# Kernel tuning notes

Measured on AMD Instinct MI355X. Metric: run time of the kernel, lower is better.

Reference implementation:

```python
import jax, jax.numpy as jnp
import numpy as np

B, S, D = 4, 2048, 1024
H, DK, DV = 16, 64, 64


def setup_inputs() -> dict:
    key = jax.random.key(0)
    ks = jax.random.split(key, 9)
    std = 1.0 / np.sqrt(D)
    inp = {
        "x": jax.random.normal(ks[0], (B, S, D), jnp.float32),
        "c": jax.random.normal(ks[1], (B, S, D), jnp.float32),
        "Wq_x": jax.random.normal(ks[2], (D, H * DK), jnp.float32) * std,
        "Wk_x": jax.random.normal(ks[3], (D, H * DK), jnp.float32) * std,
        "Wv_x": jax.random.normal(ks[4], (D, H * DV), jnp.float32) * std,
        "Wq_c": jax.random.normal(ks[5], (D, H * DK), jnp.float32) * std,
        "Wk_c": jax.random.normal(ks[6], (D, H * DK), jnp.float32) * std,
        "Wv_c": jax.random.normal(ks[7], (D, H * DV), jnp.float32) * std,
        "W_proj": jax.random.normal(ks[8], (2 * H * DV, D), jnp.float32) * (1.0 / np.sqrt(2 * H * DV)),
        "b_proj": jnp.zeros((D,), jnp.float32),
    }
    return inp


def _heads(t, hd):
    # [B,S,H*hd] -> [B,H,S,hd]
    b, s, _ = t.shape
    return t.reshape(b, s, H, hd).transpose(0, 2, 1, 3)


def reference(x, c, Wq_x, Wk_x, Wv_x, Wq_c, Wk_c, Wv_c, W_proj, b_proj):
    q = jnp.concatenate([_heads(x @ Wq_x, DK), _heads(c @ Wq_c, DK)], axis=-1)  # [B,H,S,2DK]
    k = jnp.concatenate([_heads(x @ Wk_x, DK), _heads(c @ Wk_c, DK)], axis=-1)
    v = jnp.concatenate([_heads(x @ Wv_x, DV), _heads(c @ Wv_c, DV)], axis=-1)  # [B,H,S,2DV]
    # NOTE: original scales by sqrt(k_dim), not sqrt(2*k_dim) (faithful)
    scores = jnp.einsum("bhqd,bhkd->bhqk", q, k) / np.float32(np.sqrt(DK))
    attn = jax.nn.softmax(scores, axis=-1)
    out = jnp.einsum("bhqk,bhkd->bhqd", attn, v)  # [B,H,S,2DV]
    out = out.transpose(0, 2, 1, 3).reshape(x.shape[0], x.shape[1], -1)  # [B,S,H*2DV]
    return out @ W_proj + b_proj
```

## Files before the change

kernel.cpp:

```cpp
#include <hip/hip_runtime.h>
#include <hip/hip_bf16.h>
#include <stdint.h>

#define BB 4
#define SS 2048
#define DD 1024
#define HH 16
#define DHH 128

typedef __bf16 bf16x8 __attribute__((ext_vector_type(8)));
typedef __bf16 bf16x4 __attribute__((ext_vector_type(4)));
typedef float  f32x4  __attribute__((ext_vector_type(4)));

#define GLOAD_LDS16(gp, lp) \
  __builtin_amdgcn_global_load_lds((const __attribute__((address_space(1))) unsigned int*)(gp), \
                                   (__attribute__((address_space(3))) unsigned int*)(lp), 16, 0, 0)

__global__ void cast2_kernel(const float* __restrict__ x, const float* __restrict__ c,
                             __bf16* __restrict__ out, int n) {
    int i = (blockIdx.x * blockDim.x + threadIdx.x) * 4;
    const float* src = (i < n) ? (x + i) : (c + (i - n));
    f32x4 v = *(const f32x4*)src;
    bf16x4 o;
    o[0] = (__bf16)v[0]; o[1] = (__bf16)v[1]; o[2] = (__bf16)v[2]; o[3] = (__bf16)v[3];
    *(bf16x4*)(out + i) = o;
}

__global__ void transpose_cast_kernel(const float* __restrict__ in, __bf16* __restrict__ out,
                                      int K, int N) {
    __shared__ float tile[32][33];
    int n0 = blockIdx.x * 32, k0 = blockIdx.y * 32;
    int tx = threadIdx.x, ty = threadIdx.y;
    #pragma unroll
    for (int i = 0; i < 32; i += 8)
        tile[ty + i][tx] = in[(size_t)(k0 + ty + i) * N + n0 + tx];
    __syncthreads();
    #pragma unroll
    for (int i = 0; i < 32; i += 8)
        out[(size_t)(n0 + ty + i) * K + k0 + tx] = (__bf16)tile[tx][ty + i];
}

__global__ void transpose6_kernel(const float* s0, const float* s1, const float* s2,
                                  const float* s3, const float* s4, const float* s5,
                                  __bf16* __restrict__ dst) {
    const float* srcs[6] = {s0, s1, s2, s3, s4, s5};
    const float* __restrict__ in = srcs[blockIdx.z];
    __bf16* __restrict__ out = dst + (size_t)blockIdx.z * 1024 * 1024;
    __shared__ float tile[32][33];
    int n0 = blockIdx.x * 32, k0 = blockIdx.y * 32;
    int tx = threadIdx.x, ty = threadIdx.y;
    #pragma unroll
    for (int i = 0; i < 32; i += 8)
        tile[ty + i][tx] = in[(size_t)(k0 + ty + i) * 1024 + n0 + tx];
    __syncthreads();
    #pragma unroll
    for (int i = 0; i < 32; i += 8)
        out[(size_t)(n0 + ty + i) * 1024 + k0 + tx] = (__bf16)tile[tx][ty + i];
}

template <int EPI>
__global__ void gemm128_kernel(const __bf16* __restrict__ A, const __bf16* __restrict__ Bt,
                               int K, void* __restrict__ outp, int qkv_off,
                               const float* __restrict__ bias) {
    __shared__ __bf16 As[128][32];
    __shared__ __bf16 Bs[128][32];
    const int t = threadIdx.x;
    const int wave = t >> 6, lane = t & 63;
    const int l15 = lane & 15, quad = lane >> 4;
    const int wm = (wave & 1) * 64, wn = (wave >> 1) * 64;
    const int m0 = blockIdx.x * 128, n0 = blockIdx.y * 128;
    const int lrow = lane >> 2;
    const int lcol = (lane & 3) * 8;

    f32x4 acc[4][4] = {};

    for (int k0 = 0; k0 < K; k0 += 32) {
        #pragma unroll
        for (int c2 = 0; c2 < 2; ++c2) {
            int rb = (wave * 2 + c2) * 16;
            GLOAD_LDS16(A  + (size_t)(m0 + rb + lrow) * K + k0 + lcol, &As[rb][0]);
            GLOAD_LDS16(Bt + (size_t)(n0 + rb + lrow) * K + k0 + lcol, &Bs[rb][0]);
        }
        __syncthreads();
        bf16x8 af[4], bfv[4];
        #pragma unroll
        for (int i = 0; i < 4; ++i) af[i]  = *(const bf16x8*)&As[wm + i * 16 + l15][quad * 8];
        #pragma unroll
        for (int i = 0; i < 4; ++i) bfv[i] = *(const bf16x8*)&Bs[wn + i * 16 + l15][quad * 8];
        #pragma unroll
        for (int mi = 0; mi < 4; ++mi)
            #pragma unroll
            for (int ni = 0; ni < 4; ++ni)
                acc[mi][ni] = __builtin_amdgcn_mfma_f32_16x16x32_bf16(af[mi], bfv[ni], acc[mi][ni], 0, 0, 0);
        __syncthreads();
    }

    #pragma unroll
    for (int mi = 0; mi < 4; ++mi) {
        #pragma unroll
        for (int ni = 0; ni < 4; ++ni) {
            #pragma unroll
            for (int rr = 0; rr < 4; ++rr) {
                int m = m0 + wm + mi * 16 + quad * 4 + rr;
                int n = n0 + wn + ni * 16 + l15;
                if (EPI == 0) {
                    int b = m >> 11, s = m & (SS - 1);
                    int h = n >> 6,  d = (n & 63) + qkv_off;
                    __bf16* q = (__bf16*)outp;
                    q[(((size_t)b * HH + h) * SS + s) * DHH + d] = (__bf16)acc[mi][ni][rr];
                } else if (EPI == 1) {
                    float* o = (float*)outp;
                    o[(size_t)m * 1024 + n] = acc[mi][ni][rr] + bias[n];
                } else if (EPI == 2) {
                    int h = m >> 6, dl = m & 63;
                    int b = n >> 11, s = n & (SS - 1);
                    __bf16* vt = (__bf16*)outp;
                    vt[(((size_t)b * HH + h) * DHH + dl + qkv_off) * SS + s] = (__bf16)acc[mi][ni][rr];
                } else {
                    int b = m >> 11, s = m & (SS - 1);
                    int h = n >> 6,  d = (n & 63) + qkv_off;
                    int dsw = (((d >> 3) ^ (s & 15)) << 3) | (d & 7);
                    __bf16* kq = (__bf16*)outp;
                    kq[(((size_t)b * HH + h) * SS + s) * DHH + dsw] = (__bf16)acc[mi][ni][rr];
                }
            }
        }
    }
}

#define LDS_VT 16384
#define LDS_PS 32768
__global__ __launch_bounds__(256, 2)
void attn_kernel(const __bf16* __restrict__ Q, const __bf16* __restrict__ Kg,
                 const __bf16* __restrict__ Vg, __bf16* __restrict__ O) {
    __shared__ __align__(16) char smem[49152];

    const int t = threadIdx.x;
    const int wave = t >> 6, lane = t & 63;
    const int l15 = lane & 15, quad = lane >> 4;
    const int bh = blockIdx.y;
    const int b = bh >> 4, h = bh & 15;
    const int mt = blockIdx.x;
    const size_t base  = (size_t)bh * SS * DHH;
    const size_t vbase = (size_t)bh * DHH * SS;

    int kaddr[4];
    #pragma unroll
    for (int kst = 0; kst < 4; ++kst)
        kaddr[kst] = l15 * 256 + (((4 * kst + quad) ^ l15) & 15) * 16;
    int vaddr[2];
    #pragma unroll
    for (int kst = 0; kst < 2; ++kst)
        vaddr[kst] = LDS_VT + l15 * 128 + (((4 * kst + quad) ^ (l15 & 7)) & 7) * 16;
    int prad[2];
    #pragma unroll
    for (int kst = 0; kst < 2; ++kst)
        prad[kst] = LDS_PS + (wave * 32 + l15) * 128 + (((4 * kst + quad) ^ (2 * (l15 >> 2))) & 7) * 16;
    int pwad[4];
    #pragma unroll
    for (int ns = 0; ns < 4; ++ns)
        pwad[ns] = LDS_PS + (wave * 32 + quad * 4) * 128 +
                   (((2 * ns + (l15 >> 3)) ^ (2 * quad)) & 7) * 16 + (l15 & 7) * 2;

    const __bf16* kstage = Kg + base + (size_t)wave * 2048 + lane * 8;
    const __bf16* vstage = Vg + vbase + (size_t)(wave * 32 + (lane >> 3)) * SS
                           + ((lane & 7) ^ ((lane >> 3) & 7)) * 8;

    bf16x8 qf[2][4];
    #pragma unroll
    for (int ms = 0; ms < 2; ++ms) {
        int row = mt * 128 + wave * 32 + ms * 16 + l15;
        #pragma unroll
        for (int kst = 0; kst < 4; ++kst)
            qf[ms][kst] = *(const bf16x8*)(Q + base + (size_t)row * DHH + kst * 32 + quad * 8);
    }

    f32x4 oacc[2][8] = {};
    float li_[2][4] = {};

    const float SL2E = 0.125f * 1.44269504088896f;

    for (int kt = 0; kt < SS / 64; ++kt) {
        #pragma unroll
        for (int i = 0; i < 4; ++i)
            GLOAD_LDS16(kstage + (size_t)kt * 8192 + i * 512,
                        smem + wave * 4096 + i * 1024);
        #pragma unroll
        for (int i = 0; i < 4; ++i)
            GLOAD_LDS16(vstage + kt * 64 + (size_t)i * 8 * SS,
                        smem + LDS_VT + wave * 4096 + i * 1024);
        __syncthreads();

        f32x4 sc[2][4] = {};
        #pragma unroll
        for (int kst = 0; kst < 4; ++kst) {
            bf16x8 kf[4];
            #pragma unroll
            for (int ns = 0; ns < 4; ++ns)
                kf[ns] = *(const bf16x8*)(smem + kaddr[kst] + 4096 * ns);
            #pragma unroll
            for (int ms = 0; ms < 2; ++ms)
                #pragma unroll
                for (int ns = 0; ns < 4; ++ns)
                    sc[ms][ns] = __builtin_amdgcn_mfma_f32_16x16x32_bf16(qf[ms][kst], kf[ns], sc[ms][ns], 0, 0, 0);
        }

        #pragma unroll
        for (int ms = 0; ms < 2; ++ms)
            #pragma unroll
            for (int ns = 0; ns < 4; ++ns)
                #pragma unroll
                for (int rr = 0; rr < 4; ++rr) {
                    float p = exp2f(sc[ms][ns][rr] * SL2E);
                    li_[ms][rr] += p;
                    *(__bf16*)(smem + pwad[ns] + 2048 * ms + 128 * rr) = (__bf16)p;
                }

        #pragma unroll
        for (int kst = 0; kst < 2; ++kst) {
            bf16x8 pa[2];
            #pragma unroll
            for (int ms = 0; ms < 2; ++ms)
                pa[ms] = *(const bf16x8*)(smem + prad[kst] + 2048 * ms);
            #pragma unroll
            for (int ds = 0; ds < 8; ++ds) {
                bf16x8 vf = *(const bf16x8*)(smem + vaddr[kst] + 2048 * ds);
                #pragma unroll
                for (int ms = 0; ms < 2; ++ms)
                    oacc[ms][ds] = __builtin_amdgcn_mfma_f32_16x16x32_bf16(pa[ms], vf, oacc[ms][ds], 0, 0, 0);
            }
        }
        __syncthreads();
    }

    #pragma unroll
    for (int ms = 0; ms < 2; ++ms)
        #pragma unroll
        for (int rr = 0; rr < 4; ++rr) {
            float v = li_[ms][rr];
            v += __shfl_xor(v, 1);
            v += __shfl_xor(v, 2);
            v += __shfl_xor(v, 4);
            v += __shfl_xor(v, 8);
            li_[ms][rr] = 1.f / v;
        }

    #pragma unroll
    for (int ms = 0; ms < 2; ++ms)
        #pragma unroll
        for (int rr = 0; rr < 4; ++rr) {
            int s = mt * 128 + wave * 32 + ms * 16 + quad * 4 + rr;
            size_t ob = ((size_t)b * SS + s) * (HH * DHH) + (size_t)h * DHH;
            #pragma unroll
            for (int ds = 0; ds < 8; ++ds)
                O[ob + ds * 16 + l15] = (__bf16)(oacc[ms][ds][rr] * li_[ms][rr]);
        }
}

extern "C" void kernel_launch(void* const* d_in, const int* in_sizes, int n_in,
                              void* d_out, int out_size, void* d_ws, size_t ws_size,
                              hipStream_t stream) {
    const float* x      = (const float*)d_in[0];
    const float* c      = (const float*)d_in[1];
    const float* Wq_x   = (const float*)d_in[2];
    const float* Wk_x   = (const float*)d_in[3];
    const float* Wv_x   = (const float*)d_in[4];
    const float* Wq_c   = (const float*)d_in[5];
    const float* Wk_c   = (const float*)d_in[6];
    const float* Wv_c   = (const float*)d_in[7];
    const float* W_proj = (const float*)d_in[8];
    const float* b_proj = (const float*)d_in[9];

    const size_t nXC  = (size_t)BB * SS * DD;
    const size_t nW   = (size_t)DD * DD;
    const size_t nWP  = (size_t)(2 * HH * 64) * DD;
    const size_t nQKV = (size_t)BB * HH * SS * DHH;

    __bf16* ws  = (__bf16*)d_ws;
    __bf16* xb  = ws;
    __bf16* cb  = xb + nXC;
    __bf16* wt0 = cb + nXC;
    __bf16* wt1 = wt0 + nW;
    __bf16* wt2 = wt1 + nW;
    __bf16* wt3 = wt2 + nW;
    __bf16* wt4 = wt3 + nW;
    __bf16* wt5 = wt4 + nW;
    __bf16* wtp = wt5 + nW;
    __bf16* Qb  = wtp + nWP;
    __bf16* Kb  = Qb + nQKV;
    __bf16* Vb  = Kb + nQKV;
    __bf16* Ob  = xb;

    cast2_kernel<<<(int)(2 * nXC / 1024), 256, 0, stream>>>(x, c, xb, (int)nXC);

    transpose6_kernel<<<dim3(32, 32, 6), dim3(32, 8), 0, stream>>>(
        Wq_x, Wk_x, Wv_x, Wq_c, Wk_c, Wv_c, wt0);
    transpose_cast_kernel<<<dim3(32, 64), dim3(32, 8), 0, stream>>>(W_proj, wtp, 2048, 1024);

    dim3 gg(64, 8);
    gemm128_kernel<0><<<gg, 256, 0, stream>>>(xb, wt0, 1024, Qb, 0,  nullptr);
    gemm128_kernel<0><<<gg, 256, 0, stream>>>(cb, wt3, 1024, Qb, 64, nullptr);
    gemm128_kernel<3><<<gg, 256, 0, stream>>>(xb, wt1, 1024, Kb, 0,  nullptr);
    gemm128_kernel<3><<<gg, 256, 0, stream>>>(cb, wt4, 1024, Kb, 64, nullptr);
    dim3 gv(8, 64);
    gemm128_kernel<2><<<gv, 256, 0, stream>>>(wt2, xb, 1024, Vb, 0,  nullptr);
    gemm128_kernel<2><<<gv, 256, 0, stream>>>(wt5, cb, 1024, Vb, 64, nullptr);

    attn_kernel<<<dim3(16, 64), 256, 0, stream>>>(Qb, Kb, Vb, Ob);

    gemm128_kernel<1><<<dim3(64, 8), 256, 0, stream>>>(Ob, wtp, 2048, d_out, 0, b_proj);
}
```

Before: 556.0 us.

## Fuse Q and K projections into one GEMM, prescale Q, shrink attention LDS

```diff
diff --git a/kernel.cpp b/kernel.cpp
--- a/kernel.cpp
+++ b/kernel.cpp
@@ -11,6 +11,8 @@
 typedef __bf16 bf16x8 __attribute__((ext_vector_type(8)));
 typedef __bf16 bf16x4 __attribute__((ext_vector_type(4)));
 typedef float  f32x4  __attribute__((ext_vector_type(4)));
+
+#define SL2E 0.180336880111186f
 
 #define GLOAD_LDS16(gp, lp) \
   __builtin_amdgcn_global_load_lds((const __attribute__((address_space(1))) unsigned int*)(gp), \
@@ -95,6 +97,7 @@
         __syncthreads();
     }
 
+    const size_t nQKV = (size_t)BB * HH * SS * DHH;
     #pragma unroll
     for (int mi = 0; mi < 4; ++mi) {
         #pragma unroll
@@ -103,12 +106,7 @@
             for (int rr = 0; rr < 4; ++rr) {
                 int m = m0 + wm + mi * 16 + quad * 4 + rr;
                 int n = n0 + wn + ni * 16 + l15;
-                if (EPI == 0) {
-                    int b = m >> 11, s = m & (SS - 1);
-                    int h = n >> 6,  d = (n & 63) + qkv_off;
-                    __bf16* q = (__bf16*)outp;
-                    q[(((size_t)b * HH + h) * SS + s) * DHH + d] = (__bf16)acc[mi][ni][rr];
-                } else if (EPI == 1) {
+                if (EPI == 1) {
                     float* o = (float*)outp;
                     o[(size_t)m * 1024 + n] = acc[mi][ni][rr] + bias[n];
                 } else if (EPI == 2) {
@@ -118,10 +116,16 @@
                     vt[(((size_t)b * HH + h) * DHH + dl + qkv_off) * SS + s] = (__bf16)acc[mi][ni][rr];
                 } else {
                     int b = m >> 11, s = m & (SS - 1);
-                    int h = n >> 6,  d = (n & 63) + qkv_off;
-                    int dsw = (((d >> 3) ^ (s & 15)) << 3) | (d & 7);
-                    __bf16* kq = (__bf16*)outp;
-                    kq[(((size_t)b * HH + h) * SS + s) * DHH + dsw] = (__bf16)acc[mi][ni][rr];
+                    int n1 = n & 1023;
+                    int h = n1 >> 6, d = (n1 & 63) + qkv_off;
+                    if (n < 1024) {
+                        __bf16* q = (__bf16*)outp;
+                        q[(((size_t)b * HH + h) * SS + s) * DHH + d] = (__bf16)(acc[mi][ni][rr] * SL2E);
+                    } else {
+                        int dsw = (((d >> 3) ^ (s & 15)) << 3) | (d & 7);
+                        __bf16* kq = (__bf16*)outp + nQKV;
+                        kq[(((size_t)b * HH + h) * SS + s) * DHH + dsw] = (__bf16)acc[mi][ni][rr];
+                    }
                 }
             }
         }
@@ -129,11 +133,10 @@
 }
 
 #define LDS_VT 16384
-#define LDS_PS 32768
 __global__ __launch_bounds__(256, 2)
 void attn_kernel(const __bf16* __restrict__ Q, const __bf16* __restrict__ Kg,
                  const __bf16* __restrict__ Vg, __bf16* __restrict__ O) {
-    __shared__ __align__(16) char smem[49152];
+    __shared__ __align__(16) char smem[32768];
 
     const int t = threadIdx.x;
     const int wave = t >> 6, lane = t & 63;
@@ -155,11 +158,11 @@
     int prad[2];
     #pragma unroll
     for (int kst = 0; kst < 2; ++kst)
-        prad[kst] = LDS_PS + (wave * 32 + l15) * 128 + (((4 * kst + quad) ^ (2 * (l15 >> 2))) & 7) * 16;
+        prad[kst] = (wave * 32 + l15) * 128 + (((4 * kst + quad) ^ (2 * (l15 >> 2))) & 7) * 16;
     int pwad[4];
     #pragma unroll
     for (int ns = 0; ns < 4; ++ns)
-        pwad[ns] = LDS_PS + (wave * 32 + quad * 4) * 128 +
+        pwad[ns] = (wave * 32 + quad * 4) * 128 +
                    (((2 * ns + (l15 >> 3)) ^ (2 * quad)) & 7) * 16 + (l15 & 7) * 2;
 
     const __bf16* kstage = Kg + base + (size_t)wave * 2048 + lane * 8;
@@ -177,8 +180,6 @@
 
     f32x4 oacc[2][8] = {};
     float li_[2][4] = {};
-
-    const float SL2E = 0.125f * 1.44269504088896f;
 
     for (int kt = 0; kt < SS / 64; ++kt) {
         #pragma unroll
@@ -211,10 +212,19 @@
             for (int ns = 0; ns < 4; ++ns)
                 #pragma unroll
                 for (int rr = 0; rr < 4; ++rr) {
-                    float p = exp2f(sc[ms][ns][rr] * SL2E);
+                    float p = exp2f(sc[ms][ns][rr]);
                     li_[ms][rr] += p;
-                    *(__bf16*)(smem + pwad[ns] + 2048 * ms + 128 * rr) = (__bf16)p;
+                    sc[ms][ns][rr] = p;
                 }
+        __syncthreads();
+
+        #pragma unroll
+        for (int ms = 0; ms < 2; ++ms)
+            #pragma unroll
+            for (int ns = 0; ns < 4; ++ns)
+                #pragma unroll
+                for (int rr = 0; rr < 4; ++rr)
+                    *(__bf16*)(smem + pwad[ns] + 2048 * ms + 128 * rr) = (__bf16)sc[ms][ns][rr];
 
         #pragma unroll
         for (int kst = 0; kst < 2; ++kst) {
@@ -280,12 +290,10 @@
     __bf16* xb  = ws;
     __bf16* cb  = xb + nXC;
     __bf16* wt0 = cb + nXC;
-    __bf16* wt1 = wt0 + nW;
-    __bf16* wt2 = wt1 + nW;
-    __bf16* wt3 = wt2 + nW;
-    __bf16* wt4 = wt3 + nW;
-    __bf16* wt5 = wt4 + nW;
-    __bf16* wtp = wt5 + nW;
+    __bf16* wt2 = wt0 + 2 * nW;
+    __bf16* wt3 = wt0 + 3 * nW;
+    __bf16* wt5 = wt0 + 5 * nW;
+    __bf16* wtp = wt0 + 6 * nW;
     __bf16* Qb  = wtp + nWP;
     __bf16* Kb  = Qb + nQKV;
     __bf16* Vb  = Kb + nQKV;
@@ -297,11 +305,9 @@
         Wq_x, Wk_x, Wv_x, Wq_c, Wk_c, Wv_c, wt0);
     transpose_cast_kernel<<<dim3(32, 64), dim3(32, 8), 0, stream>>>(W_proj, wtp, 2048, 1024);
 
-    dim3 gg(64, 8);
-    gemm128_kernel<0><<<gg, 256, 0, stream>>>(xb, wt0, 1024, Qb, 0,  nullptr);
-    gemm128_kernel<0><<<gg, 256, 0, stream>>>(cb, wt3, 1024, Qb, 64, nullptr);
-    gemm128_kernel<3><<<gg, 256, 0, stream>>>(xb, wt1, 1024, Kb, 0,  nullptr);
-    gemm128_kernel<3><<<gg, 256, 0, stream>>>(cb, wt4, 1024, Kb, 64, nullptr);
+    dim3 gqk(64, 16);
+    gemm128_kernel<4><<<gqk, 256, 0, stream>>>(xb, wt0, 1024, Qb, 0,  nullptr);
+    gemm128_kernel<4><<<gqk, 256, 0, stream>>>(cb, wt3, 1024, Qb, 64, nullptr);
     dim3 gv(8, 64);
     gemm128_kernel<2><<<gv, 256, 0, stream>>>(wt2, xb, 1024, Vb, 0,  nullptr);
     gemm128_kernel<2><<<gv, 256, 0, stream>>>(wt5, cb, 1024, Vb, 64, nullptr);
```

New measurement: 520.2 us. 6.4% less time.
